# Kernel optimization log

Measured on AMD Instinct MI355X. Metric: run time of the kernel, lower is better.

The kernel has to match this reference:

```python
import jax, jax.numpy as jnp
import numpy as np

N_NODES = 200_000
N_EDGES = 400_000
EMB_DIM = 128
HID_DIM = 24
N_TYPES = 8


def setup_inputs() -> dict:
    key = jax.random.key(0)
    k_emb, k_src, k_typ, k_w1, k_w2 = jax.random.split(key, 5)
    rgcn_emb = jax.random.normal(k_emb, (N_NODES, EMB_DIM), dtype=jnp.float32)
    edge_index = jax.random.randint(k_src, (2, N_EDGES), 0, N_NODES, dtype=jnp.int32)
    edge_type = jax.random.randint(k_typ, (N_EDGES,), 0, N_TYPES, dtype=jnp.int32)
    # per-edge-type 2-layer MLP params: Linear(2D->H), Linear(H->1)
    W1 = jax.random.normal(k_w1, (N_TYPES, 2 * EMB_DIM, HID_DIM), dtype=jnp.float32) * 0.05
    b1 = jnp.zeros((N_TYPES, HID_DIM), dtype=jnp.float32)
    W2 = jax.random.normal(k_w2, (N_TYPES, HID_DIM), dtype=jnp.float32) * 0.05
    b2 = jnp.zeros((N_TYPES,), dtype=jnp.float32)
    return {"rgcn_emb": rgcn_emb, "edge_index": edge_index, "edge_type": edge_type,
            "W1": W1, "b1": b1, "W2": W2, "b2": b2}


def reference(rgcn_emb, edge_index, edge_type, W1, b1, W2, b2):
    src, dst = edge_index[0], edge_index[1]
    # gather + concat: [E, 2D]
    edge_emb = jnp.concatenate([rgcn_emb[src], rgcn_emb[dst]], axis=-1)
    # dense per-type expert compute, then select by routing (MoE-style)
    h = jnp.einsum('ed,tdh->teh', edge_emb, W1) + b1[:, None, :]  # [T,E,H]
    h = jnp.where(h > 0, h, 0.01 * h)  # LeakyReLU(0.01)
    s = jnp.einsum('teh,th->te', h, W2) + b2[:, None]  # [T,E]
    onehot = jax.nn.one_hot(edge_type, N_TYPES, dtype=s.dtype)  # [E,T]
    scores = jnp.einsum('te,et->e', s, onehot)  # scatter-select per edge
    return (scores, rgcn_emb)
```

## Files before the change

kernel.cpp:

```cpp
#include <hip/hip_runtime.h>


typedef _Float16 h2 __attribute__((ext_vector_type(2)));
typedef float    f4 __attribute__((ext_vector_type(4)));

constexpr int N_NODES = 200000;
constexpr int N_EDGES = 400000;
constexpr int EMB_DIM = 128;
constexpr int HID     = 24;
constexpr int N_TYPES = 8;
constexpr int BLK     = 256;

constexpr int MAX_PAD      = N_EDGES + N_TYPES * (BLK - 1);
constexpr int SCORE_BLOCKS = (MAX_PAD + BLK - 1) / BLK;
constexpr int SC_BLOCKS    = 128;
constexpr int SC_CH        = (N_EDGES + SC_BLOCKS - 1) / SC_BLOCKS;

constexpr int PREP_HIST   = 64;
constexpr int PREP_W1     = 16;
constexpr int PREP_CONV   = 1968;
constexpr int PREP_BLOCKS = PREP_HIST + PREP_W1 + PREP_CONV;

constexpr size_t SORT_BYTES  = (size_t)(16 + MAX_PAD) * sizeof(int);
constexpr size_t EMB16_OFF   = (SORT_BYTES + 255) & ~(size_t)255;
constexpr size_t EMB16_BYTES = (size_t)N_NODES * EMB_DIM * 2;
constexpr size_t W16_OFF     = EMB16_OFF + EMB16_BYTES;
constexpr size_t W16_BYTES   = (size_t)N_TYPES * 128 * HID * 4;
constexpr size_t NEED16      = W16_OFF + W16_BYTES;

__device__ __forceinline__ float fdot2f(h2 a, h2 b, float c) {
#if __has_builtin(__builtin_amdgcn_fdot2)
    return __builtin_amdgcn_fdot2(a, b, c, false);
#else
    return c + (float)a[0] * (float)b[0] + (float)a[1] * (float)b[1];
#endif
}

__global__ __launch_bounds__(BLK) void prep_k(
        const int* __restrict__ etype, int* __restrict__ counts,
        const float* __restrict__ emb, float* __restrict__ out,
        int2* __restrict__ emb16, const float* __restrict__ W1,
        h2* __restrict__ w16) {
    int b = blockIdx.x;
    if (b < PREP_HIST) {
        __shared__ int lc[N_TYPES];
        if (threadIdx.x < N_TYPES) lc[threadIdx.x] = 0;
        __syncthreads();
        const int4* et4 = (const int4*)etype;
        for (int g = b * BLK + threadIdx.x; g < N_EDGES / 4; g += PREP_HIST * BLK) {
            int4 v = et4[g];
            atomicAdd(&lc[v.x], 1); atomicAdd(&lc[v.y], 1);
            atomicAdd(&lc[v.z], 1); atomicAdd(&lc[v.w], 1);
        }
        __syncthreads();
        if (threadIdx.x < N_TYPES) {
            int v = lc[threadIdx.x];
            if (v) atomicAdd(&counts[threadIdx.x], v);
        }
    } else if (b < PREP_HIST + PREP_W1) {
        int cb = b - PREP_HIST;
        for (int p = cb * BLK + threadIdx.x; p < N_TYPES * 128 * HID; p += PREP_W1 * BLK) {
            int t   = p / (128 * HID);
            int rem = p - t * 128 * HID;
            int kp  = rem / HID, j = rem - kp * HID;
            h2 v;
            v[0] = (_Float16)W1[(t * 256 + 2 * kp)     * HID + j];
            v[1] = (_Float16)W1[(t * 256 + 2 * kp + 1) * HID + j];
            w16[p] = v;
        }
    } else {
        int cb = b - PREP_HIST - PREP_W1;
        const f4* in4 = (const f4*)emb;
        f4* o4 = (f4*)(out + N_EDGES);
        const int n4 = N_NODES * EMB_DIM / 4;
        for (int i = cb * BLK + threadIdx.x; i < n4; i += PREP_CONV * BLK) {
            f4 a = __builtin_nontemporal_load(&in4[i]);
            __builtin_nontemporal_store(a, &o4[i]);
            union { int2 v; h2 h[2]; } u;
            u.h[0] = h2{(_Float16)a.x, (_Float16)a.y};
            u.h[1] = h2{(_Float16)a.z, (_Float16)a.w};
            emb16[i] = u.v;
        }
    }
}

__global__ __launch_bounds__(BLK) void scatter_k(
        const int* __restrict__ etype, int* __restrict__ counts,
        int* __restrict__ sorted) {
    __shared__ int lc[N_TYPES], base[N_TYPES];
    int b = blockIdx.x;
    if (threadIdx.x < N_TYPES) lc[threadIdx.x] = 0;
    __syncthreads();
    int e0 = b * SC_CH, e1 = min(e0 + SC_CH, N_EDGES);
    for (int e = e0 + threadIdx.x; e < e1; e += BLK)
        atomicAdd(&lc[etype[e]], 1);
    __syncthreads();
    if (threadIdx.x < N_TYPES)
        base[threadIdx.x] = atomicAdd(&counts[8 + threadIdx.x], lc[threadIdx.x]);
    __syncthreads();
    if (threadIdx.x < N_TYPES) lc[threadIdx.x] = 0;
    __syncthreads();
    int poff[N_TYPES];
    int off = 0;
#pragma unroll
    for (int t = 0; t < N_TYPES; ++t) {
        poff[t] = off;
        off += ((counts[t] + BLK - 1) / BLK) * BLK;
    }
    for (int e = e0 + threadIdx.x; e < e1; e += BLK) {
        int t = etype[e];
        int r = atomicAdd(&lc[t], 1);
        sorted[poff[t] + base[t] + r] = e;
    }
}

__device__ __forceinline__ void compute_chunk(const int4* __restrict__ r,
                                              const h2* __restrict__ wrow,
                                              float acc[HID]) {
    const h2* hp = (const h2*)r;
#pragma unroll
    for (int kp = 0; kp < 32; ++kp) {
#pragma unroll
        for (int j = 0; j < HID; ++j)
            acc[j] = fdot2f(hp[kp], wrow[kp * HID + j], acc[j]);
    }
}

__global__ __launch_bounds__(BLK) void score16_ns_k(
        const unsigned short* __restrict__ emb16u,
        const int* __restrict__ srci, const int* __restrict__ dsti,
        const int* __restrict__ counts, const int* __restrict__ sorted,
        const h2* __restrict__ w16, const float* __restrict__ b1,
        const float* __restrict__ W2, const float* __restrict__ b2,
        float* __restrict__ out) {
    int poff[N_TYPES];
    int off = 0;
#pragma unroll
    for (int t = 0; t < N_TYPES; ++t) {
        poff[t] = off;
        off += ((counts[t] + BLK - 1) / BLK) * BLK;
    }
    int slot0 = blockIdx.x * BLK;
    if (slot0 >= off) return;
    int t = 0;
#pragma unroll
    for (int i = 1; i < N_TYPES; ++i)
        if (slot0 >= poff[i]) t = i;
    t = __builtin_amdgcn_readfirstlane(t);
    int cnt = counts[t];
    int local = slot0 - poff[t] + (int)threadIdx.x;
    if (local >= cnt) return;
    int e = sorted[slot0 + threadIdx.x];
    int s = srci[e], d = dsti[e];

    float acc[HID];
#pragma unroll
    for (int j = 0; j < HID; ++j) acc[j] = b1[t * HID + j];
    const h2* wt = w16 + (size_t)t * 128 * HID;
    const int4* x0 = (const int4*)(emb16u + (size_t)s * EMB_DIM);
    const int4* x1 = (const int4*)(emb16u + (size_t)d * EMB_DIM);

    int4 A[8], B[8];
#pragma unroll
    for (int k = 0; k < 8; ++k) A[k] = x0[k];
#pragma unroll
    for (int k = 0; k < 8; ++k) B[k] = x0[8 + k];
    compute_chunk(A, wt + 0 * 32 * HID, acc);
#pragma unroll
    for (int k = 0; k < 8; ++k) A[k] = x1[k];
    compute_chunk(B, wt + 1 * 32 * HID, acc);
#pragma unroll
    for (int k = 0; k < 8; ++k) B[k] = x1[8 + k];
    compute_chunk(A, wt + 2 * 32 * HID, acc);
    compute_chunk(B, wt + 3 * 32 * HID, acc);

    float sc = b2[t];
#pragma unroll
    for (int j = 0; j < HID; ++j) {
        float h = acc[j];
        h = (h > 0.f) ? h : 0.01f * h;
        sc = fmaf(h, W2[t * HID + j], sc);
    }
    out[e] = sc;
}

__global__ __launch_bounds__(BLK) void fallback_k(
        const float* __restrict__ emb,
        const int* __restrict__ srci, const int* __restrict__ dsti,
        const int* __restrict__ etype,
        const float* __restrict__ W1, const float* __restrict__ b1,
        const float* __restrict__ W2, const float* __restrict__ b2,
        float* __restrict__ out) {
    long long i0 = (long long)blockIdx.x * BLK + threadIdx.x;
    const float4* s4 = (const float4*)emb;
    float4* o4 = (float4*)(out + N_EDGES);
    const long long n4 = (long long)N_NODES * EMB_DIM / 4;
    for (long long i = i0; i < n4; i += (long long)gridDim.x * BLK)
        o4[i] = s4[i];
    for (int e = (int)i0; e < N_EDGES; e += gridDim.x * BLK) {
        int t = etype[e];
        int s = srci[e], d = dsti[e];
        float acc[HID];
#pragma unroll
        for (int j = 0; j < HID; ++j) acc[j] = b1[t * HID + j];
        const float* w = W1 + (size_t)t * 2 * EMB_DIM * HID;
        for (int k = 0; k < EMB_DIM; ++k) {
            float x = emb[(size_t)s * EMB_DIM + k];
#pragma unroll
            for (int j = 0; j < HID; ++j) acc[j] = fmaf(x, w[k * HID + j], acc[j]);
        }
        for (int k = 0; k < EMB_DIM; ++k) {
            float x = emb[(size_t)d * EMB_DIM + k];
#pragma unroll
            for (int j = 0; j < HID; ++j) acc[j] = fmaf(x, w[(EMB_DIM + k) * HID + j], acc[j]);
        }
        float sc = b2[t];
#pragma unroll
        for (int j = 0; j < HID; ++j) {
            float h = acc[j];
            h = (h > 0.f) ? h : 0.01f * h;
            sc = fmaf(h, W2[t * HID + j], sc);
        }
        out[e] = sc;
    }
}

extern "C" void kernel_launch(void* const* d_in, const int* in_sizes, int n_in,
                              void* d_out, int out_size, void* d_ws, size_t ws_size,
                              hipStream_t stream) {
    const float* emb   = (const float*)d_in[0];
    const int*   eidx  = (const int*)d_in[1];
    const int*   etype = (const int*)d_in[2];
    const float* W1    = (const float*)d_in[3];
    const float* b1    = (const float*)d_in[4];
    const float* W2    = (const float*)d_in[5];
    const float* b2    = (const float*)d_in[6];
    float* out = (float*)d_out;
    const int* srci = eidx;
    const int* dsti = eidx + N_EDGES;

    if (ws_size >= NEED16) {
        int* counts = (int*)d_ws;
        int* sorted = counts + 16;
        int2* emb16 = (int2*)((char*)d_ws + EMB16_OFF);
        h2*   w16   = (h2*)((char*)d_ws + W16_OFF);
        (void)hipMemsetAsync(counts, 0, 16 * sizeof(int), stream);
        prep_k<<<PREP_BLOCKS, BLK, 0, stream>>>(etype, counts, emb, out, emb16, W1, w16);
        scatter_k<<<SC_BLOCKS, BLK, 0, stream>>>(etype, counts, sorted);
        score16_ns_k<<<SCORE_BLOCKS, BLK, 0, stream>>>(
            (const unsigned short*)emb16, srci, dsti, counts, sorted,
            w16, b1, W2, b2, out);
    } else {
        fallback_k<<<2048, BLK, 0, stream>>>(emb, srci, dsti, etype, W1, b1, W2, b2, out);
    }
}
```

Measured before the change: 287.0 us.

## Replace atomic histogram with per-chunk counts and overlap emb copy with scoring

Per-chunk type histograms are written to workspace instead of being combined with global atomics. The scatter kernel then computes a deterministic prefix over chunks, which removes the memset and the atomic base allocation. The fp32 embedding passthrough copy moves out of the prep kernel into extra blocks of the scoring kernel, so the bandwidth-bound copy can overlap the compute-bound scoring. The cost is a serial 128-entry prefix loop in every scatter block and a larger grid for the scoring launch.

```diff
diff --git a/kernel.cpp b/kernel.cpp
--- a/kernel.cpp
+++ b/kernel.cpp
@@ -11,21 +11,26 @@
 constexpr int N_TYPES = 8;
 constexpr int BLK     = 256;
 
-constexpr int MAX_PAD      = N_EDGES + N_TYPES * (BLK - 1);
+constexpr int CHUNKS  = 128;
+constexpr int CH_SZ   = N_EDGES / CHUNKS;
+constexpr int MAX_PAD = N_EDGES + N_TYPES * (BLK - 1);
 constexpr int SCORE_BLOCKS = (MAX_PAD + BLK - 1) / BLK;
-constexpr int SC_BLOCKS    = 128;
-constexpr int SC_CH        = (N_EDGES + SC_BLOCKS - 1) / SC_BLOCKS;
-
-constexpr int PREP_HIST   = 64;
-constexpr int PREP_W1     = 16;
-constexpr int PREP_CONV   = 1968;
+constexpr int COPY_BLOCKS  = 1024;
+
+constexpr int PREP_HIST = CHUNKS;
+constexpr int PREP_W1   = 16;
+constexpr int PREP_CONV = 1024;
 constexpr int PREP_BLOCKS = PREP_HIST + PREP_W1 + PREP_CONV;
 
-constexpr size_t SORT_BYTES  = (size_t)(16 + MAX_PAD) * sizeof(int);
+constexpr int OFF_CC     = 0;
+constexpr int OFF_COUNTS = OFF_CC + CHUNKS * N_TYPES;
+constexpr int OFF_POFF   = OFF_COUNTS + N_TYPES;
+constexpr int OFF_SORTED = OFF_POFF + N_TYPES;
+constexpr size_t SORT_BYTES  = (size_t)(OFF_SORTED + MAX_PAD) * sizeof(int);
 constexpr size_t EMB16_OFF   = (SORT_BYTES + 255) & ~(size_t)255;
 constexpr size_t EMB16_BYTES = (size_t)N_NODES * EMB_DIM * 2;
 constexpr size_t W16_OFF     = EMB16_OFF + EMB16_BYTES;
-constexpr size_t W16_BYTES   = (size_t)N_TYPES * 128 * HID * 4;
+constexpr size_t W16_BYTES   = (size_t)N_TYPES * 128 * HID * sizeof(int);
 constexpr size_t NEED16      = W16_OFF + W16_BYTES;
 
 __device__ __forceinline__ float fdot2f(h2 a, h2 b, float c) {
@@ -37,26 +42,20 @@
 }
 
 __global__ __launch_bounds__(BLK) void prep_k(
-        const int* __restrict__ etype, int* __restrict__ counts,
-        const float* __restrict__ emb, float* __restrict__ out,
-        int2* __restrict__ emb16, const float* __restrict__ W1,
-        h2* __restrict__ w16) {
+        const int* __restrict__ etype, int* __restrict__ ws,
+        const float* __restrict__ emb, int2* __restrict__ emb16,
+        const float* __restrict__ W1, h2* __restrict__ w16) {
     int b = blockIdx.x;
     if (b < PREP_HIST) {
         __shared__ int lc[N_TYPES];
         if (threadIdx.x < N_TYPES) lc[threadIdx.x] = 0;
         __syncthreads();
-        const int4* et4 = (const int4*)etype;
-        for (int g = b * BLK + threadIdx.x; g < N_EDGES / 4; g += PREP_HIST * BLK) {
-            int4 v = et4[g];
-            atomicAdd(&lc[v.x], 1); atomicAdd(&lc[v.y], 1);
-            atomicAdd(&lc[v.z], 1); atomicAdd(&lc[v.w], 1);
-        }
+        int e0 = b * CH_SZ;
+        for (int e = e0 + (int)threadIdx.x; e < e0 + CH_SZ; e += BLK)
+            atomicAdd(&lc[etype[e]], 1);
         __syncthreads();
-        if (threadIdx.x < N_TYPES) {
-            int v = lc[threadIdx.x];
-            if (v) atomicAdd(&counts[threadIdx.x], v);
-        }
+        if (threadIdx.x < N_TYPES)
+            ws[OFF_CC + b * N_TYPES + threadIdx.x] = lc[threadIdx.x];
     } else if (b < PREP_HIST + PREP_W1) {
         int cb = b - PREP_HIST;
         for (int p = cb * BLK + threadIdx.x; p < N_TYPES * 128 * HID; p += PREP_W1 * BLK) {
@@ -71,11 +70,9 @@
     } else {
         int cb = b - PREP_HIST - PREP_W1;
         const f4* in4 = (const f4*)emb;
-        f4* o4 = (f4*)(out + N_EDGES);
         const int n4 = N_NODES * EMB_DIM / 4;
         for (int i = cb * BLK + threadIdx.x; i < n4; i += PREP_CONV * BLK) {
-            f4 a = __builtin_nontemporal_load(&in4[i]);
-            __builtin_nontemporal_store(a, &o4[i]);
+            f4 a = in4[i];
             union { int2 v; h2 h[2]; } u;
             u.h[0] = h2{(_Float16)a.x, (_Float16)a.y};
             u.h[1] = h2{(_Float16)a.z, (_Float16)a.w};
@@ -85,32 +82,57 @@
 }
 
 __global__ __launch_bounds__(BLK) void scatter_k(
-        const int* __restrict__ etype, int* __restrict__ counts,
-        int* __restrict__ sorted) {
-    __shared__ int lc[N_TYPES], base[N_TYPES];
+        const int* __restrict__ etype, int* __restrict__ ws) {
+    __shared__ int sbase[N_TYPES];
+    __shared__ int tot[N_TYPES];
+    __shared__ int mybase[N_TYPES];
+    __shared__ int spoff[N_TYPES];
+    __shared__ int lc[N_TYPES];
     int b = blockIdx.x;
-    if (threadIdx.x < N_TYPES) lc[threadIdx.x] = 0;
+    if (threadIdx.x < N_TYPES) {
+        int t = threadIdx.x, s = 0, mb = 0;
+        for (int c = 0; c < CHUNKS; ++c) {
+            if (c == b) mb = s;
+            s += ws[OFF_CC + c * N_TYPES + t];
+        }
+        tot[t] = s;
+        mybase[t] = mb;
+        lc[t] = 0;
+    }
     __syncthreads();
-    int e0 = b * SC_CH, e1 = min(e0 + SC_CH, N_EDGES);
-    for (int e = e0 + threadIdx.x; e < e1; e += BLK)
-        atomicAdd(&lc[etype[e]], 1);
+    if (threadIdx.x == 0) {
+        int off = 0;
+        for (int t = 0; t < N_TYPES; ++t) {
+            spoff[t] = off;
+            off += ((tot[t] + BLK - 1) / BLK) * BLK;
+        }
+    }
     __syncthreads();
-    if (threadIdx.x < N_TYPES)
-        base[threadIdx.x] = atomicAdd(&counts[8 + threadIdx.x], lc[threadIdx.x]);
+    if (threadIdx.x < N_TYPES) {
+        sbase[threadIdx.x] = spoff[threadIdx.x] + mybase[threadIdx.x];
+        if (b == 0) {
+            ws[OFF_COUNTS + threadIdx.x] = tot[threadIdx.x];
+            ws[OFF_POFF + threadIdx.x]   = spoff[threadIdx.x];
+        }
+    }
     __syncthreads();
-    if (threadIdx.x < N_TYPES) lc[threadIdx.x] = 0;
-    __syncthreads();
-    int poff[N_TYPES];
-    int off = 0;
-#pragma unroll
-    for (int t = 0; t < N_TYPES; ++t) {
-        poff[t] = off;
-        off += ((counts[t] + BLK - 1) / BLK) * BLK;
-    }
-    for (int e = e0 + threadIdx.x; e < e1; e += BLK) {
+    int e0 = b * CH_SZ;
+    int* sorted = ws + OFF_SORTED;
+    for (int e = e0 + (int)threadIdx.x; e < e0 + CH_SZ; e += BLK) {
         int t = etype[e];
         int r = atomicAdd(&lc[t], 1);
-        sorted[poff[t] + base[t] + r] = e;
+        sorted[sbase[t] + r] = e;
+    }
+}
+
+__device__ __forceinline__ void do_copy(const float* __restrict__ emb,
+                                        float* __restrict__ out, int cb, int nb) {
+    const f4* s4 = (const f4*)emb;
+    f4* o4 = (f4*)(out + N_EDGES);
+    const int n4 = N_NODES * EMB_DIM / 4;
+    for (int i = cb * BLK + (int)threadIdx.x; i < n4; i += nb * BLK) {
+        f4 a = s4[i];
+        __builtin_nontemporal_store(a, &o4[i]);
     }
 }
 
@@ -126,21 +148,26 @@
     }
 }
 
-__global__ __launch_bounds__(BLK) void score16_ns_k(
-        const unsigned short* __restrict__ emb16u,
+__global__ __launch_bounds__(BLK) void score16_k(
+        const unsigned short* __restrict__ emb16u, const float* __restrict__ emb,
         const int* __restrict__ srci, const int* __restrict__ dsti,
-        const int* __restrict__ counts, const int* __restrict__ sorted,
+        const int* __restrict__ ws,
         const h2* __restrict__ w16, const float* __restrict__ b1,
         const float* __restrict__ W2, const float* __restrict__ b2,
         float* __restrict__ out) {
-    int poff[N_TYPES];
-    int off = 0;
+    int b = blockIdx.x;
+    if (b >= SCORE_BLOCKS) {
+        do_copy(emb, out, b - SCORE_BLOCKS, (int)gridDim.x - SCORE_BLOCKS);
+        return;
+    }
+    int poff[N_TYPES], counts[N_TYPES];
 #pragma unroll
     for (int t = 0; t < N_TYPES; ++t) {
-        poff[t] = off;
-        off += ((counts[t] + BLK - 1) / BLK) * BLK;
-    }
-    int slot0 = blockIdx.x * BLK;
+        counts[t] = ws[OFF_COUNTS + t];
+        poff[t]   = ws[OFF_POFF + t];
+    }
+    int off = poff[N_TYPES - 1] + ((counts[N_TYPES - 1] + BLK - 1) / BLK) * BLK;
+    int slot0 = b * BLK;
     if (slot0 >= off) return;
     int t = 0;
 #pragma unroll
@@ -150,6 +177,7 @@
     int cnt = counts[t];
     int local = slot0 - poff[t] + (int)threadIdx.x;
     if (local >= cnt) return;
+    const int* sorted = ws + OFF_SORTED;
     int e = sorted[slot0 + threadIdx.x];
     int s = srci[e], d = dsti[e];
 
@@ -192,8 +220,8 @@
         const float* __restrict__ W2, const float* __restrict__ b2,
         float* __restrict__ out) {
     long long i0 = (long long)blockIdx.x * BLK + threadIdx.x;
-    const float4* s4 = (const float4*)emb;
-    float4* o4 = (float4*)(out + N_EDGES);
+    const f4* s4 = (const f4*)emb;
+    f4* o4 = (f4*)(out + N_EDGES);
     const long long n4 = (long long)N_NODES * EMB_DIM / 4;
     for (long long i = i0; i < n4; i += (long long)gridDim.x * BLK)
         o4[i] = s4[i];
@@ -240,15 +268,13 @@
     const int* dsti = eidx + N_EDGES;
 
     if (ws_size >= NEED16) {
-        int* counts = (int*)d_ws;
-        int* sorted = counts + 16;
+        int*  ws    = (int*)d_ws;
         int2* emb16 = (int2*)((char*)d_ws + EMB16_OFF);
         h2*   w16   = (h2*)((char*)d_ws + W16_OFF);
-        (void)hipMemsetAsync(counts, 0, 16 * sizeof(int), stream);
-        prep_k<<<PREP_BLOCKS, BLK, 0, stream>>>(etype, counts, emb, out, emb16, W1, w16);
-        scatter_k<<<SC_BLOCKS, BLK, 0, stream>>>(etype, counts, sorted);
-        score16_ns_k<<<SCORE_BLOCKS, BLK, 0, stream>>>(
-            (const unsigned short*)emb16, srci, dsti, counts, sorted,
+        prep_k<<<PREP_BLOCKS, BLK, 0, stream>>>(etype, ws, emb, emb16, W1, w16);
+        scatter_k<<<CHUNKS, BLK, 0, stream>>>(etype, ws);
+        score16_k<<<SCORE_BLOCKS + COPY_BLOCKS, BLK, 0, stream>>>(
+            (const unsigned short*)emb16, emb, srci, dsti, ws,
             w16, b1, W2, b2, out);
     } else {
         fallback_k<<<2048, BLK, 0, stream>>>(emb, srci, dsti, etype, W1, b1, W2, b2, out);
```

Result: no change. 283.4 us (-1.2%).
